# Kernel optimization log

Hardware: AMD Instinct MI355X
Metric: run time of the kernel (lower is better)

The kernel has to match this reference:

```python
import jax, jax.numpy as jnp
import numpy as np

B, S, D = 2, 2048, 1024
H = 16
HS = D // H  # head_size = 64
SCALE = HS ** 0.5


def setup_inputs() -> dict:
    key = jax.random.key(0)
    ks = jax.random.split(key, 7)
    std = 1.0 / np.sqrt(D)
    return {
        "x": jax.random.normal(ks[0], (B, S, D), dtype=jnp.float32),
        "Wq": jax.random.normal(ks[1], (D, D), dtype=jnp.float32) * std,
        "bq": jax.random.normal(ks[2], (D,), dtype=jnp.float32) * std,
        "Wk": jax.random.normal(ks[3], (D, D), dtype=jnp.float32) * std,
        "bk": jax.random.normal(ks[4], (D,), dtype=jnp.float32) * std,
        "Wv": jax.random.normal(ks[5], (D, D), dtype=jnp.float32) * std,
        "bv": jax.random.normal(ks[6], (D,), dtype=jnp.float32) * std,
    }


def reference(x, Wq, bq, Wk, bk, Wv, bv):
    bs, seq, _ = x.shape
    # QKV projections (torch Linear: x @ W.T + b)
    Q = (x @ Wq.T + bq).reshape(bs, seq, H, HS)
    K = (x @ Wk.T + bk).reshape(bs, seq, H, HS)
    V = (x @ Wv.T + bv).reshape(bs, seq, H, HS)
    # scores[b,h,q,k] = Q . K / scale
    scores = jnp.einsum("bqhd,bkhd->bhqk", Q, K) / SCALE
    # causal mask: disallow k > q
    causal = jnp.triu(jnp.ones((seq, seq), dtype=bool), k=1)
    scores = jnp.where(causal, -jnp.inf, scores)
    probs = jax.nn.softmax(scores, axis=-1)
    att = jnp.einsum("bhqk,bkhd->bqhd", probs, V)
    return att.reshape(bs, seq, H * HS)
```

## Files before the change

### kernel.cpp

```cpp
#include <hip/hip_runtime.h>

typedef unsigned short ushort_t;
typedef __bf16 bf16x8 __attribute__((ext_vector_type(8)));
typedef unsigned short ushortx8 __attribute__((ext_vector_type(8)));
typedef unsigned short ushortx4 __attribute__((ext_vector_type(4)));
typedef unsigned int uintx4 __attribute__((ext_vector_type(4)));
typedef float floatx4 __attribute__((ext_vector_type(4)));

__device__ inline void load16_lds(const ushort_t* g, ushort_t* l) {
  __builtin_amdgcn_global_load_lds(
      (__attribute__((address_space(1))) void*)(g),
      (__attribute__((address_space(3))) void*)(l),
      16, 0, 0);
}

__device__ inline float bf2f(ushort_t u) {
  unsigned int v = ((unsigned int)u) << 16;
  return __builtin_bit_cast(float, v);
}

__device__ inline ushort_t f2bf(float f) {
  unsigned int u = __builtin_bit_cast(unsigned int, f);
  u += 0x7fffu + ((u >> 16) & 1u);
  return (ushort_t)(u >> 16);
}

__device__ inline bf16x8 ldfrag(const ushort_t* p) {
  return __builtin_bit_cast(bf16x8, *(const ushortx8*)p);
}

__device__ inline bool sniff_f32(const ushort_t* x, int lane_off) {
  float v = fabsf(bf2f(x[lane_off]));
  bool big = !(v < 1e4f);
  return __ballot(big) != 0ull;
}

__global__ __launch_bounds__(256) void convert_all(
    const void* __restrict__ x,
    const void* __restrict__ wq, const void* __restrict__ wk, const void* __restrict__ wv,
    const void* __restrict__ bq, const void* __restrict__ bk, const void* __restrict__ bv,
    ushort_t* __restrict__ xb, ushort_t* __restrict__ wqb,
    ushort_t* __restrict__ wkb, ushort_t* __restrict__ wvb,
    float* __restrict__ biasf, int* __restrict__ flag)
{
  const bool f32 = sniff_f32((const ushort_t*)x, (int)(threadIdx.x & 63));
  const int seg = blockIdx.y;
  if (seg == 4) {
    if (blockIdx.x == 0 && threadIdx.x == 0) *flag = f32 ? 1 : 0;
    const int i = blockIdx.x * 256 + threadIdx.x;
    if (i >= 1024) return;
    const void* bs[3] = {bq, bk, bv};
#pragma unroll
    for (int k = 0; k < 3; ++k)
      biasf[k * 1024 + i] = f32 ? ((const float*)bs[k])[i] : bf2f(((const ushort_t*)bs[k])[i]);
    return;
  }
  const void* src = (seg == 0) ? x : (seg == 1) ? wq : (seg == 2) ? wk : wv;
  ushort_t* dst   = (seg == 0) ? xb : (seg == 1) ? wqb : (seg == 2) ? wkb : wvb;
  const int n = (seg == 0) ? 4194304 : 1048576;
  const int i = (blockIdx.x * 256 + threadIdx.x) * 8;
  if (i >= n) return;
  if (f32) {
    const float* s = (const float*)src + i;
    ushortx8 o;
#pragma unroll
    for (int j = 0; j < 8; ++j) o[j] = f2bf(s[j]);
    *(ushortx8*)(dst + i) = o;
  } else {
    *(ushortx8*)(dst + i) = *(const ushortx8*)((const ushort_t*)src + i);
  }
}

__global__ __launch_bounds__(256, 2) void qkv_gemm(
    const ushort_t* __restrict__ x,
    const ushort_t* __restrict__ Wq, const ushort_t* __restrict__ Wk,
    const ushort_t* __restrict__ Wv, const float* __restrict__ biasf,
    ushort_t* __restrict__ Qo, ushort_t* __restrict__ Ko, ushort_t* __restrict__ Vt)
{
  __shared__ __attribute__((aligned(16))) ushort_t As[128 * 32];
  __shared__ __attribute__((aligned(16))) ushort_t Bs[128 * 32];

  const int which = blockIdx.z;
  const ushort_t* W = (which == 0) ? Wq : (which == 1) ? Wk : Wv;
  const float oscale = (which == 0) ? 0.18033688011112042f : 1.0f;

  const int n0 = blockIdx.x * 128;
  const int m0 = blockIdx.y * 128;

  const int tid  = threadIdx.x;
  const int wave = tid >> 6;
  const int lane = tid & 63;
  const int ln   = lane & 15;
  const int quad = lane >> 4;
  const int wm = (wave >> 1) * 64;
  const int wn = (wave & 1) * 64;

  floatx4 acc[4][4];
#pragma unroll
  for (int i = 0; i < 4; ++i)
#pragma unroll
    for (int j = 0; j < 4; ++j) acc[i][j] = floatx4{0.f, 0.f, 0.f, 0.f};

  const int c1 = tid, c2 = tid + 256;
  const ushort_t* ga1 = x + (m0 + (c1 >> 2)) * 1024 + (c1 & 3) * 8;
  const ushort_t* ga2 = x + (m0 + (c2 >> 2)) * 1024 + (c2 & 3) * 8;
  const ushort_t* gb1 = W + (n0 + (c1 >> 2)) * 1024 + (c1 & 3) * 8;
  const ushort_t* gb2 = W + (n0 + (c2 >> 2)) * 1024 + (c2 & 3) * 8;
  ushort_t* la1 = As + wave * 512;
  ushort_t* la2 = As + 2048 + wave * 512;
  ushort_t* lb1 = Bs + wave * 512;
  ushort_t* lb2 = Bs + 2048 + wave * 512;

  for (int kt = 0; kt < 1024; kt += 32) {
    __syncthreads();
    load16_lds(ga1 + kt, la1);
    load16_lds(ga2 + kt, la2);
    load16_lds(gb1 + kt, lb1);
    load16_lds(gb2 + kt, lb2);
    __syncthreads();

    bf16x8 af[4], bfr[4];
#pragma unroll
    for (int mi = 0; mi < 4; ++mi)
      af[mi] = ldfrag(As + (wm + mi * 16 + ln) * 32 + quad * 8);
#pragma unroll
    for (int ni = 0; ni < 4; ++ni)
      bfr[ni] = ldfrag(Bs + (wn + ni * 16 + ln) * 32 + quad * 8);
#pragma unroll
    for (int mi = 0; mi < 4; ++mi)
#pragma unroll
      for (int ni = 0; ni < 4; ++ni)
        acc[mi][ni] = __builtin_amdgcn_mfma_f32_16x16x32_bf16(af[mi], bfr[ni], acc[mi][ni], 0, 0, 0);
  }

  float bvv[4];
#pragma unroll
  for (int ni = 0; ni < 4; ++ni) bvv[ni] = biasf[which * 1024 + n0 + wn + ni * 16 + ln];

  if (which == 2) {
#pragma unroll
    for (int mi = 0; mi < 4; ++mi)
#pragma unroll
      for (int ni = 0; ni < 4; ++ni) {
        const int col = n0 + wn + ni * 16 + ln;
        const int row0 = m0 + wm + mi * 16 + quad * 4;
        const int b = row0 >> 11, s0 = row0 & 2047;
        const int h = col >> 6, hs = col & 63;
        ushortx4 pk;
#pragma unroll
        for (int r = 0; r < 4; ++r) pk[r] = f2bf(acc[mi][ni][r] + bvv[ni]);
        *(ushortx4*)(Vt + ((size_t)((b * 16 + h) * 64 + hs)) * 2048 + s0) = pk;
      }
  } else {
    ushort_t* out = (which == 0) ? Qo : Ko;
#pragma unroll
    for (int mi = 0; mi < 4; ++mi)
#pragma unroll
      for (int ni = 0; ni < 4; ++ni) {
        const int col = n0 + wn + ni * 16 + ln;
#pragma unroll
        for (int r = 0; r < 4; ++r) {
          const int row = m0 + wm + mi * 16 + quad * 4 + r;
          out[row * 1024 + col] = f2bf((acc[mi][ni][r] + bvv[ni]) * oscale);
        }
      }
  }
}

__global__ __launch_bounds__(128) void flash8(
    const ushort_t* __restrict__ Q, const ushort_t* __restrict__ Kx,
    const ushort_t* __restrict__ Vt, void* __restrict__ out,
    const int* __restrict__ flag)
{
  __shared__ __attribute__((aligned(16))) float Cb[64][68];
  __shared__ float lbuf[64][4];

  const bool f32o = (*flag != 0);
  const int tid  = threadIdx.x;
  const int wave = tid >> 6;
  const int lane = tid & 63;
  const int ln = lane & 15, quad = lane >> 4;

  const int idxA = (ln + 32 * (quad & 1)) * 4;
  const int idxB = idxA + 64;
  const bool hiq = (quad >> 1) != 0;

  const int i = blockIdx.x;
  const int xcd = i & 7, j = i >> 3;
  const int bh = xcd * 4 + (j & 3);
  const int cc = 31 - (j >> 2);
  const int b = bh >> 4, h = bh & 15;
  const int qw = cc * 64;
  const int ntiles = cc + 1;

  const ushort_t* kbase = Kx + ((size_t)b * 2048) * 1024 + h * 64;
  const ushort_t* vbase = Vt + (size_t)bh * 64 * 2048;

  bf16x8 qf[4][2];
#pragma unroll
  for (int bi = 0; bi < 4; ++bi)
#pragma unroll
    for (int ks = 0; ks < 2; ++ks)
      qf[bi][ks] = ldfrag(Q + (size_t)(b * 2048 + qw + bi * 16 + ln) * 1024 + h * 64 + ks * 32 + quad * 8);

  floatx4 ot[4][4];
#pragma unroll
  for (int ai = 0; ai < 4; ++ai)
#pragma unroll
    for (int bi = 0; bi < 4; ++bi) ot[ai][bi] = floatx4{0.f, 0.f, 0.f, 0.f};
  float li[4] = {0.f, 0.f, 0.f, 0.f};

  for (int t = wave; t < ntiles; t += 2) {
    const int kv0 = t * 64;
    const bool diag = (t == ntiles - 1);

    const ushort_t* kp = kbase + (size_t)(kv0 + ln) * 1024 + quad * 8;
    bf16x8 kf[4][2];
#pragma unroll
    for (int mi = 0; mi < 4; ++mi)
#pragma unroll
      for (int ks = 0; ks < 2; ++ks)
        kf[mi][ks] = ldfrag(kp + mi * 16 * 1024 + ks * 32);

    const ushort_t* vp = vbase + (size_t)ln * 2048 + kv0 + quad * 8;
    bf16x8 vf[4][2];
#pragma unroll
    for (int ai = 0; ai < 4; ++ai)
#pragma unroll
      for (int ks = 0; ks < 2; ++ks)
        vf[ai][ks] = ldfrag(vp + ai * 16 * 2048 + ks * 32);

#pragma unroll
    for (int bi = 0; bi < 4; ++bi) {
      floatx4 st[4];
#pragma unroll
      for (int mi = 0; mi < 4; ++mi) st[mi] = floatx4{0.f, 0.f, 0.f, 0.f};
#pragma unroll
      for (int mi = 0; mi < 4; ++mi) {
        st[mi] = __builtin_amdgcn_mfma_f32_16x16x32_bf16(kf[mi][0], qf[bi][0], st[mi], 0, 0, 0);
        st[mi] = __builtin_amdgcn_mfma_f32_16x16x32_bf16(kf[mi][1], qf[bi][1], st[mi], 0, 0, 0);
      }

      const int qrow = qw + bi * 16 + ln;
      float p[4][4];
      if (diag) {
#pragma unroll
        for (int mi = 0; mi < 4; ++mi)
#pragma unroll
          for (int r = 0; r < 4; ++r) {
            const int kv = kv0 + mi * 16 + quad * 4 + r;
            const float e = __builtin_amdgcn_exp2f(st[mi][r]);
            p[mi][r] = (kv > qrow) ? 0.f : e;
          }
      } else {
#pragma unroll
        for (int mi = 0; mi < 4; ++mi)
#pragma unroll
          for (int r = 0; r < 4; ++r) p[mi][r] = __builtin_amdgcn_exp2f(st[mi][r]);
      }

      unsigned d[4][2];
#pragma unroll
      for (int mi = 0; mi < 4; ++mi) {
        li[bi] += (p[mi][0] + p[mi][1]) + (p[mi][2] + p[mi][3]);
        d[mi][0] = __builtin_amdgcn_perm(
            __builtin_bit_cast(unsigned, p[mi][1]), __builtin_bit_cast(unsigned, p[mi][0]), 0x07060302u);
        d[mi][1] = __builtin_amdgcn_perm(
            __builtin_bit_cast(unsigned, p[mi][3]), __builtin_bit_cast(unsigned, p[mi][2]), 0x07060302u);
      }

      bf16x8 pb[2];
#pragma unroll
      for (int ks = 0; ks < 2; ++ks) {
        uintx4 w;
#pragma unroll
        for (int jj = 0; jj < 4; ++jj) {
          const int idx = (jj >> 1) ? idxB : idxA;
          const int lo = __builtin_amdgcn_ds_bpermute(idx, (int)d[2 * ks][jj & 1]);
          const int hi = __builtin_amdgcn_ds_bpermute(idx, (int)d[2 * ks + 1][jj & 1]);
          w[jj] = (unsigned)(hiq ? hi : lo);
        }
        pb[ks] = __builtin_bit_cast(bf16x8, w);
      }

#pragma unroll
      for (int ai = 0; ai < 4; ++ai) {
        ot[ai][bi] = __builtin_amdgcn_mfma_f32_16x16x32_bf16(vf[ai][0], pb[0], ot[ai][bi], 0, 0, 0);
        ot[ai][bi] = __builtin_amdgcn_mfma_f32_16x16x32_bf16(vf[ai][1], pb[1], ot[ai][bi], 0, 0, 0);
      }
    }
  }

  if (wave == 1) {
#pragma unroll
    for (int bi = 0; bi < 4; ++bi) {
#pragma unroll
      for (int ai = 0; ai < 4; ++ai)
        *(floatx4*)&Cb[bi * 16 + ln][ai * 16 + quad * 4] = ot[ai][bi];
      lbuf[bi * 16 + ln][quad] = 0.f;
    }
#pragma unroll
    for (int bi = 0; bi < 4; ++bi) lbuf[lane][bi] = li[bi];
  }
  __syncthreads();
  if (wave == 0) {
#pragma unroll
    for (int bi = 0; bi < 4; ++bi) {
#pragma unroll
      for (int ai = 0; ai < 4; ++ai) {
        const floatx4 o = *(const floatx4*)&Cb[bi * 16 + ln][ai * 16 + quad * 4];
#pragma unroll
        for (int r = 0; r < 4; ++r) ot[ai][bi][r] += o[r];
      }
      li[bi] += lbuf[lane][bi];
    }

#pragma unroll
    for (int bi = 0; bi < 4; ++bi) {
      li[bi] += __shfl_xor(li[bi], 16);
      li[bi] += __shfl_xor(li[bi], 32);
      const float inv = 1.0f / li[bi];
      const int qrow = qw + bi * 16 + ln;
      if (f32o) {
        float* of = (float*)out;
#pragma unroll
        for (int ai = 0; ai < 4; ++ai) {
          floatx4 o;
#pragma unroll
          for (int r = 0; r < 4; ++r) o[r] = ot[ai][bi][r] * inv;
          *(floatx4*)(of + (size_t)(b * 2048 + qrow) * 1024 + h * 64 + ai * 16 + quad * 4) = o;
        }
      } else {
        ushort_t* ob = (ushort_t*)out;
#pragma unroll
        for (int ai = 0; ai < 4; ++ai) {
          ushortx4 pk;
#pragma unroll
          for (int r = 0; r < 4; ++r) pk[r] = f2bf(ot[ai][bi][r] * inv);
          *(ushortx4*)(ob + (size_t)(b * 2048 + qrow) * 1024 + h * 64 + ai * 16 + quad * 4) = pk;
        }
      }
    }
  }
}

extern "C" void kernel_launch(void* const* d_in, const int* in_sizes, int n_in,
                              void* d_out, int out_size, void* d_ws, size_t ws_size,
                              hipStream_t stream) {
  char* w = (char*)d_ws;
  int* flag = (int*)w;
  size_t off = 256;
  ushort_t* xb  = (ushort_t*)(w + off); off += (size_t)4194304 * 2;
  ushort_t* wqb = (ushort_t*)(w + off); off += (size_t)1048576 * 2;
  ushort_t* wkb = (ushort_t*)(w + off); off += (size_t)1048576 * 2;
  ushort_t* wvb = (ushort_t*)(w + off); off += (size_t)1048576 * 2;
  float* biasf  = (float*)(w + off);    off += (size_t)3 * 1024 * 4;
  ushort_t* Qw  = (ushort_t*)(w + off); off += (size_t)4194304 * 2;
  ushort_t* Kw  = (ushort_t*)(w + off); off += (size_t)4194304 * 2;
  ushort_t* Vtw = (ushort_t*)(w + off);

  convert_all<<<dim3(2048, 5), 256, 0, stream>>>(
      d_in[0], d_in[1], d_in[3], d_in[5], d_in[2], d_in[4], d_in[6],
      xb, wqb, wkb, wvb, biasf, flag);
  qkv_gemm<<<dim3(8, 32, 3), 256, 0, stream>>>(xb, wqb, wkb, wvb, biasf, Qw, Kw, Vtw);
  flash8<<<1024, 128, 0, stream>>>(Qw, Kw, Vtw, d_out, flag);
}
```

Measured before the change: 161.3 us.

## Share double-buffered LDS K/V tiles across two query-block waves in flash kernel

The attention kernel now gives each 2-wave block 128 query rows (64 per wave) instead of splitting one 64-row block's KV range across two waves. K and V tiles are staged through double-buffered LDS, with the next tile's global loads issued into registers during compute. This removes the cross-wave reduction of partial outputs and halves global K/V traffic per query row. The cost is one barrier per KV tile and idle time for wave 0 on the final tile. The grid drops to 512 blocks with a new causal-balanced ordering.

```diff
diff --git a/kernel.cpp b/kernel.cpp
--- a/kernel.cpp
+++ b/kernel.cpp
@@ -167,13 +167,13 @@
   }
 }
 
-__global__ __launch_bounds__(128) void flash8(
+__global__ __launch_bounds__(128) void flash9(
     const ushort_t* __restrict__ Q, const ushort_t* __restrict__ Kx,
     const ushort_t* __restrict__ Vt, void* __restrict__ out,
     const int* __restrict__ flag)
 {
-  __shared__ __attribute__((aligned(16))) float Cb[64][68];
-  __shared__ float lbuf[64][4];
+  __shared__ __attribute__((aligned(16))) ushort_t sK[2][64 * 72];
+  __shared__ __attribute__((aligned(16))) ushort_t sV[2][64 * 72];
 
   const bool f32o = (*flag != 0);
   const int tid  = threadIdx.x;
@@ -185,13 +185,18 @@
   const int idxB = idxA + 64;
   const bool hiq = (quad >> 1) != 0;
 
+  const int rl   = (lane & 15) + 16 * ((lane >> 5) & 1);
+  const int hsel = (lane >> 4) & 1;
+
   const int i = blockIdx.x;
-  const int xcd = i & 7, j = i >> 3;
-  const int bh = xcd * 4 + (j & 3);
-  const int cc = 31 - (j >> 2);
+  const int s = (i < 256) ? (i >> 5) : ((i - 256) >> 5);
+  const int c = (i < 256) ? (15 - s) : s;
+  const int bhi = i & 31;
+  const int bh = (bhi & 7) * 4 + (bhi >> 3);
   const int b = bh >> 4, h = bh & 15;
-  const int qw = cc * 64;
-  const int ntiles = cc + 1;
+  const int qw = c * 128 + wave * 64;
+  const int ntiles = 2 * c + 2;
+  const int mytiles = 2 * c + wave;
 
   const ushort_t* kbase = Kx + ((size_t)b * 2048) * 1024 + h * 64;
   const ushort_t* vbase = Vt + (size_t)bh * 64 * 2048;
@@ -210,135 +215,140 @@
     for (int bi = 0; bi < 4; ++bi) ot[ai][bi] = floatx4{0.f, 0.f, 0.f, 0.f};
   float li[4] = {0.f, 0.f, 0.f, 0.f};
 
-  for (int t = wave; t < ntiles; t += 2) {
+  uintx4 stgK[4], stgV[4];
+  {
+    const ushort_t* kg = kbase + (size_t)(0 + 32 * wave + rl) * 1024 + hsel * 32;
+    const ushort_t* vg = vbase + (size_t)(32 * wave + rl) * 2048 + 0 + hsel * 32;
+#pragma unroll
+    for (int c16 = 0; c16 < 4; ++c16) {
+      stgK[c16] = *(const uintx4*)(kg + c16 * 8);
+      stgV[c16] = *(const uintx4*)(vg + c16 * 8);
+    }
+  }
+
+  for (int t = 0; t < ntiles; ++t) {
     const int kv0 = t * 64;
-    const bool diag = (t == ntiles - 1);
-
-    const ushort_t* kp = kbase + (size_t)(kv0 + ln) * 1024 + quad * 8;
-    bf16x8 kf[4][2];
-#pragma unroll
-    for (int mi = 0; mi < 4; ++mi)
-#pragma unroll
-      for (int ks = 0; ks < 2; ++ks)
-        kf[mi][ks] = ldfrag(kp + mi * 16 * 1024 + ks * 32);
-
-    const ushort_t* vp = vbase + (size_t)ln * 2048 + kv0 + quad * 8;
-    bf16x8 vf[4][2];
-#pragma unroll
-    for (int ai = 0; ai < 4; ++ai)
-#pragma unroll
-      for (int ks = 0; ks < 2; ++ks)
-        vf[ai][ks] = ldfrag(vp + ai * 16 * 2048 + ks * 32);
-
-#pragma unroll
-    for (int bi = 0; bi < 4; ++bi) {
-      floatx4 st[4];
-#pragma unroll
-      for (int mi = 0; mi < 4; ++mi) st[mi] = floatx4{0.f, 0.f, 0.f, 0.f};
-#pragma unroll
-      for (int mi = 0; mi < 4; ++mi) {
-        st[mi] = __builtin_amdgcn_mfma_f32_16x16x32_bf16(kf[mi][0], qf[bi][0], st[mi], 0, 0, 0);
-        st[mi] = __builtin_amdgcn_mfma_f32_16x16x32_bf16(kf[mi][1], qf[bi][1], st[mi], 0, 0, 0);
-      }
-
-      const int qrow = qw + bi * 16 + ln;
-      float p[4][4];
-      if (diag) {
-#pragma unroll
-        for (int mi = 0; mi < 4; ++mi)
-#pragma unroll
-          for (int r = 0; r < 4; ++r) {
-            const int kv = kv0 + mi * 16 + quad * 4 + r;
-            const float e = __builtin_amdgcn_exp2f(st[mi][r]);
-            p[mi][r] = (kv > qrow) ? 0.f : e;
+    const int buf = t & 1;
+
+    {
+      ushort_t* wk = sK[buf] + (32 * wave + rl) * 72 + hsel * 32;
+      ushort_t* wv = sV[buf] + (32 * wave + rl) * 72 + hsel * 32;
+#pragma unroll
+      for (int c16 = 0; c16 < 4; ++c16) {
+        *(uintx4*)(wk + c16 * 8) = stgK[c16];
+        *(uintx4*)(wv + c16 * 8) = stgV[c16];
+      }
+    }
+    __syncthreads();
+
+    if (t + 1 < ntiles) {
+      const int kvn = (t + 1) * 64;
+      const ushort_t* kg = kbase + (size_t)(kvn + 32 * wave + rl) * 1024 + hsel * 32;
+      const ushort_t* vg = vbase + (size_t)(32 * wave + rl) * 2048 + kvn + hsel * 32;
+#pragma unroll
+      for (int c16 = 0; c16 < 4; ++c16) {
+        stgK[c16] = *(const uintx4*)(kg + c16 * 8);
+        stgV[c16] = *(const uintx4*)(vg + c16 * 8);
+      }
+    }
+
+    if (t <= mytiles) {
+      const bool diag = (t == mytiles);
+
+      bf16x8 kf[4][2], vf[4][2];
+#pragma unroll
+      for (int mi = 0; mi < 4; ++mi)
+#pragma unroll
+        for (int ks = 0; ks < 2; ++ks) {
+          kf[mi][ks] = ldfrag(sK[buf] + (mi * 16 + ln) * 72 + ks * 32 + quad * 8);
+          vf[mi][ks] = ldfrag(sV[buf] + (mi * 16 + ln) * 72 + ks * 32 + quad * 8);
+        }
+
+#pragma unroll
+      for (int bi = 0; bi < 4; ++bi) {
+        floatx4 st[4];
+#pragma unroll
+        for (int mi = 0; mi < 4; ++mi) st[mi] = floatx4{0.f, 0.f, 0.f, 0.f};
+#pragma unroll
+        for (int mi = 0; mi < 4; ++mi) {
+          st[mi] = __builtin_amdgcn_mfma_f32_16x16x32_bf16(kf[mi][0], qf[bi][0], st[mi], 0, 0, 0);
+          st[mi] = __builtin_amdgcn_mfma_f32_16x16x32_bf16(kf[mi][1], qf[bi][1], st[mi], 0, 0, 0);
+        }
+
+        const int qrow = qw + bi * 16 + ln;
+        float p[4][4];
+        if (diag) {
+#pragma unroll
+          for (int mi = 0; mi < 4; ++mi)
+#pragma unroll
+            for (int r = 0; r < 4; ++r) {
+              const int kv = kv0 + mi * 16 + quad * 4 + r;
+              const float e = __builtin_amdgcn_exp2f(st[mi][r]);
+              p[mi][r] = (kv > qrow) ? 0.f : e;
+            }
+        } else {
+#pragma unroll
+          for (int mi = 0; mi < 4; ++mi)
+#pragma unroll
+            for (int r = 0; r < 4; ++r) p[mi][r] = __builtin_amdgcn_exp2f(st[mi][r]);
+        }
+
+        unsigned d[4][2];
+#pragma unroll
+        for (int mi = 0; mi < 4; ++mi) {
+          li[bi] += (p[mi][0] + p[mi][1]) + (p[mi][2] + p[mi][3]);
+          d[mi][0] = __builtin_amdgcn_perm(
+              __builtin_bit_cast(unsigned, p[mi][1]), __builtin_bit_cast(unsigned, p[mi][0]), 0x07060302u);
+          d[mi][1] = __builtin_amdgcn_perm(
+              __builtin_bit_cast(unsigned, p[mi][3]), __builtin_bit_cast(unsigned, p[mi][2]), 0x07060302u);
+        }
+
+        bf16x8 pb[2];
+#pragma unroll
+        for (int ks = 0; ks < 2; ++ks) {
+          uintx4 w;
+#pragma unroll
+          for (int jj = 0; jj < 4; ++jj) {
+            const int idx = (jj >> 1) ? idxB : idxA;
+            const int lo = __builtin_amdgcn_ds_bpermute(idx, (int)d[2 * ks][jj & 1]);
+            const int hi = __builtin_amdgcn_ds_bpermute(idx, (int)d[2 * ks + 1][jj & 1]);
+            w[jj] = (unsigned)(hiq ? hi : lo);
           }
-      } else {
-#pragma unroll
-        for (int mi = 0; mi < 4; ++mi)
-#pragma unroll
-          for (int r = 0; r < 4; ++r) p[mi][r] = __builtin_amdgcn_exp2f(st[mi][r]);
-      }
-
-      unsigned d[4][2];
-#pragma unroll
-      for (int mi = 0; mi < 4; ++mi) {
-        li[bi] += (p[mi][0] + p[mi][1]) + (p[mi][2] + p[mi][3]);
-        d[mi][0] = __builtin_amdgcn_perm(
-            __builtin_bit_cast(unsigned, p[mi][1]), __builtin_bit_cast(unsigned, p[mi][0]), 0x07060302u);
-        d[mi][1] = __builtin_amdgcn_perm(
-            __builtin_bit_cast(unsigned, p[mi][3]), __builtin_bit_cast(unsigned, p[mi][2]), 0x07060302u);
-      }
-
-      bf16x8 pb[2];
-#pragma unroll
-      for (int ks = 0; ks < 2; ++ks) {
-        uintx4 w;
-#pragma unroll
-        for (int jj = 0; jj < 4; ++jj) {
-          const int idx = (jj >> 1) ? idxB : idxA;
-          const int lo = __builtin_amdgcn_ds_bpermute(idx, (int)d[2 * ks][jj & 1]);
-          const int hi = __builtin_amdgcn_ds_bpermute(idx, (int)d[2 * ks + 1][jj & 1]);
-          w[jj] = (unsigned)(hiq ? hi : lo);
-        }
-        pb[ks] = __builtin_bit_cast(bf16x8, w);
-      }
-
+          pb[ks] = __builtin_bit_cast(bf16x8, w);
+        }
+
+#pragma unroll
+        for (int ai = 0; ai < 4; ++ai) {
+          ot[ai][bi] = __builtin_amdgcn_mfma_f32_16x16x32_bf16(vf[ai][0], pb[0], ot[ai][bi], 0, 0, 0);
+          ot[ai][bi] = __builtin_amdgcn_mfma_f32_16x16x32_bf16(vf[ai][1], pb[1], ot[ai][bi], 0, 0, 0);
+        }
+      }
+    }
+  }
+
+#pragma unroll
+  for (int bi = 0; bi < 4; ++bi) {
+    li[bi] += __shfl_xor(li[bi], 16);
+    li[bi] += __shfl_xor(li[bi], 32);
+    const float inv = 1.0f / li[bi];
+    const int qrow = qw + bi * 16 + ln;
+    if (f32o) {
+      float* of = (float*)out;
 #pragma unroll
       for (int ai = 0; ai < 4; ++ai) {
-        ot[ai][bi] = __builtin_amdgcn_mfma_f32_16x16x32_bf16(vf[ai][0], pb[0], ot[ai][bi], 0, 0, 0);
-        ot[ai][bi] = __builtin_amdgcn_mfma_f32_16x16x32_bf16(vf[ai][1], pb[1], ot[ai][bi], 0, 0, 0);
-      }
-    }
-  }
-
-  if (wave == 1) {
-#pragma unroll
-    for (int bi = 0; bi < 4; ++bi) {
-#pragma unroll
-      for (int ai = 0; ai < 4; ++ai)
-        *(floatx4*)&Cb[bi * 16 + ln][ai * 16 + quad * 4] = ot[ai][bi];
-      lbuf[bi * 16 + ln][quad] = 0.f;
-    }
-#pragma unroll
-    for (int bi = 0; bi < 4; ++bi) lbuf[lane][bi] = li[bi];
-  }
-  __syncthreads();
-  if (wave == 0) {
-#pragma unroll
-    for (int bi = 0; bi < 4; ++bi) {
+        floatx4 o;
+#pragma unroll
+        for (int r = 0; r < 4; ++r) o[r] = ot[ai][bi][r] * inv;
+        *(floatx4*)(of + (size_t)(b * 2048 + qrow) * 1024 + h * 64 + ai * 16 + quad * 4) = o;
+      }
+    } else {
+      ushort_t* ob = (ushort_t*)out;
 #pragma unroll
       for (int ai = 0; ai < 4; ++ai) {
-        const floatx4 o = *(const floatx4*)&Cb[bi * 16 + ln][ai * 16 + quad * 4];
-#pragma unroll
-        for (int r = 0; r < 4; ++r) ot[ai][bi][r] += o[r];
-      }
-      li[bi] += lbuf[lane][bi];
-    }
-
-#pragma unroll
-    for (int bi = 0; bi < 4; ++bi) {
-      li[bi] += __shfl_xor(li[bi], 16);
-      li[bi] += __shfl_xor(li[bi], 32);
-      const float inv = 1.0f / li[bi];
-      const int qrow = qw + bi * 16 + ln;
-      if (f32o) {
-        float* of = (float*)out;
-#pragma unroll
-        for (int ai = 0; ai < 4; ++ai) {
-          floatx4 o;
-#pragma unroll
-          for (int r = 0; r < 4; ++r) o[r] = ot[ai][bi][r] * inv;
-          *(floatx4*)(of + (size_t)(b * 2048 + qrow) * 1024 + h * 64 + ai * 16 + quad * 4) = o;
-        }
-      } else {
-        ushort_t* ob = (ushort_t*)out;
-#pragma unroll
-        for (int ai = 0; ai < 4; ++ai) {
-          ushortx4 pk;
-#pragma unroll
-          for (int r = 0; r < 4; ++r) pk[r] = f2bf(ot[ai][bi][r] * inv);
-          *(ushortx4*)(ob + (size_t)(b * 2048 + qrow) * 1024 + h * 64 + ai * 16 + quad * 4) = pk;
-        }
+        ushortx4 pk;
+#pragma unroll
+        for (int r = 0; r < 4; ++r) pk[r] = f2bf(ot[ai][bi][r] * inv);
+        *(ushortx4*)(ob + (size_t)(b * 2048 + qrow) * 1024 + h * 64 + ai * 16 + quad * 4) = pk;
       }
     }
   }
@@ -363,5 +373,5 @@
       d_in[0], d_in[1], d_in[3], d_in[5], d_in[2], d_in[4], d_in[6],
       xb, wqb, wkb, wvb, biasf, flag);
   qkv_gemm<<<dim3(8, 32, 3), 256, 0, stream>>>(xb, wqb, wkb, wvb, biasf, Qw, Kw, Vtw);
-  flash8<<<1024, 128, 0, stream>>>(Qw, Kw, Vtw, d_out, flag);
-}
+  flash9<<<512, 128, 0, stream>>>(Qw, Kw, Vtw, d_out, flag);
+}
```

After: 194.8 us. 20.8% more time.

## Pair causal query chunks per block and split KV tiles across four waves

Applied to the files above, without the earlier changes.

Each block now processes two 64-row query chunks in sequence, a long one (31-pr) and a short one (pr), so every block does the same amount of causal work. The grid is halved to 512 blocks. Blocks grow to 256 threads, with KV tiles strided across four waves instead of two. Partial outputs are combined through a two-level shared-memory tree reduction. This targets load imbalance and tail effects from uneven causal chunk sizes, at the cost of more barriers and fewer, larger blocks.

```diff
diff --git a/kernel.cpp b/kernel.cpp
--- a/kernel.cpp
+++ b/kernel.cpp
@@ -167,13 +167,14 @@
   }
 }
 
-__global__ __launch_bounds__(128) void flash8(
+__global__ __launch_bounds__(256) void flash10(
     const ushort_t* __restrict__ Q, const ushort_t* __restrict__ Kx,
     const ushort_t* __restrict__ Vt, void* __restrict__ out,
     const int* __restrict__ flag)
 {
-  __shared__ __attribute__((aligned(16))) float Cb[64][68];
-  __shared__ float lbuf[64][4];
+  __shared__ __attribute__((aligned(16))) float CbA[64][68];
+  __shared__ __attribute__((aligned(16))) float CbB[64][68];
+  __shared__ float lbA[64][4], lbB[64][4];
 
   const bool f32o = (*flag != 0);
   const int tid  = threadIdx.x;
@@ -188,156 +189,201 @@
   const int i = blockIdx.x;
   const int xcd = i & 7, j = i >> 3;
   const int bh = xcd * 4 + (j & 3);
-  const int cc = 31 - (j >> 2);
+  const int pr = j >> 2;
   const int b = bh >> 4, h = bh & 15;
-  const int qw = cc * 64;
-  const int ntiles = cc + 1;
 
   const ushort_t* kbase = Kx + ((size_t)b * 2048) * 1024 + h * 64;
   const ushort_t* vbase = Vt + (size_t)bh * 64 * 2048;
 
-  bf16x8 qf[4][2];
-#pragma unroll
-  for (int bi = 0; bi < 4; ++bi)
-#pragma unroll
-    for (int ks = 0; ks < 2; ++ks)
-      qf[bi][ks] = ldfrag(Q + (size_t)(b * 2048 + qw + bi * 16 + ln) * 1024 + h * 64 + ks * 32 + quad * 8);
-
-  floatx4 ot[4][4];
-#pragma unroll
-  for (int ai = 0; ai < 4; ++ai)
-#pragma unroll
-    for (int bi = 0; bi < 4; ++bi) ot[ai][bi] = floatx4{0.f, 0.f, 0.f, 0.f};
-  float li[4] = {0.f, 0.f, 0.f, 0.f};
-
-  for (int t = wave; t < ntiles; t += 2) {
-    const int kv0 = t * 64;
-    const bool diag = (t == ntiles - 1);
-
-    const ushort_t* kp = kbase + (size_t)(kv0 + ln) * 1024 + quad * 8;
-    bf16x8 kf[4][2];
-#pragma unroll
-    for (int mi = 0; mi < 4; ++mi)
+  for (int phase = 0; phase < 2; ++phase) {
+    const int c = phase ? pr : (31 - pr);
+    const int qw = c * 64;
+    const int ntiles = c + 1;
+
+    bf16x8 qf[4][2];
+#pragma unroll
+    for (int bi = 0; bi < 4; ++bi)
 #pragma unroll
       for (int ks = 0; ks < 2; ++ks)
-        kf[mi][ks] = ldfrag(kp + mi * 16 * 1024 + ks * 32);
-
-    const ushort_t* vp = vbase + (size_t)ln * 2048 + kv0 + quad * 8;
-    bf16x8 vf[4][2];
+        qf[bi][ks] = ldfrag(Q + (size_t)(b * 2048 + qw + bi * 16 + ln) * 1024 + h * 64 + ks * 32 + quad * 8);
+
+    floatx4 ot[4][4];
 #pragma unroll
     for (int ai = 0; ai < 4; ++ai)
 #pragma unroll
-      for (int ks = 0; ks < 2; ++ks)
-        vf[ai][ks] = ldfrag(vp + ai * 16 * 2048 + ks * 32);
-
-#pragma unroll
-    for (int bi = 0; bi < 4; ++bi) {
-      floatx4 st[4];
-#pragma unroll
-      for (int mi = 0; mi < 4; ++mi) st[mi] = floatx4{0.f, 0.f, 0.f, 0.f};
-#pragma unroll
-      for (int mi = 0; mi < 4; ++mi) {
-        st[mi] = __builtin_amdgcn_mfma_f32_16x16x32_bf16(kf[mi][0], qf[bi][0], st[mi], 0, 0, 0);
-        st[mi] = __builtin_amdgcn_mfma_f32_16x16x32_bf16(kf[mi][1], qf[bi][1], st[mi], 0, 0, 0);
-      }
-
-      const int qrow = qw + bi * 16 + ln;
-      float p[4][4];
-      if (diag) {
-#pragma unroll
-        for (int mi = 0; mi < 4; ++mi)
-#pragma unroll
-          for (int r = 0; r < 4; ++r) {
-            const int kv = kv0 + mi * 16 + quad * 4 + r;
-            const float e = __builtin_amdgcn_exp2f(st[mi][r]);
-            p[mi][r] = (kv > qrow) ? 0.f : e;
+      for (int bi = 0; bi < 4; ++bi) ot[ai][bi] = floatx4{0.f, 0.f, 0.f, 0.f};
+    float li[4] = {0.f, 0.f, 0.f, 0.f};
+
+    for (int t = wave; t < ntiles; t += 4) {
+      const int kv0 = t * 64;
+      const bool diag = (t == ntiles - 1);
+
+      const ushort_t* kp = kbase + (size_t)(kv0 + ln) * 1024 + quad * 8;
+      bf16x8 kf[4][2];
+#pragma unroll
+      for (int mi = 0; mi < 4; ++mi)
+#pragma unroll
+        for (int ks = 0; ks < 2; ++ks)
+          kf[mi][ks] = ldfrag(kp + mi * 16 * 1024 + ks * 32);
+
+      const ushort_t* vp = vbase + (size_t)ln * 2048 + kv0 + quad * 8;
+      bf16x8 vf[4][2];
+#pragma unroll
+      for (int ai = 0; ai < 4; ++ai)
+#pragma unroll
+        for (int ks = 0; ks < 2; ++ks)
+          vf[ai][ks] = ldfrag(vp + ai * 16 * 2048 + ks * 32);
+
+#pragma unroll
+      for (int bi = 0; bi < 4; ++bi) {
+        floatx4 st[4];
+#pragma unroll
+        for (int mi = 0; mi < 4; ++mi) st[mi] = floatx4{0.f, 0.f, 0.f, 0.f};
+#pragma unroll
+        for (int mi = 0; mi < 4; ++mi) {
+          st[mi] = __builtin_amdgcn_mfma_f32_16x16x32_bf16(kf[mi][0], qf[bi][0], st[mi], 0, 0, 0);
+          st[mi] = __builtin_amdgcn_mfma_f32_16x16x32_bf16(kf[mi][1], qf[bi][1], st[mi], 0, 0, 0);
+        }
+
+        const int qrow = qw + bi * 16 + ln;
+        float p[4][4];
+        if (diag) {
+#pragma unroll
+          for (int mi = 0; mi < 4; ++mi)
+#pragma unroll
+            for (int r = 0; r < 4; ++r) {
+              const int kv = kv0 + mi * 16 + quad * 4 + r;
+              const float e = __builtin_amdgcn_exp2f(st[mi][r]);
+              p[mi][r] = (kv > qrow) ? 0.f : e;
+            }
+        } else {
+#pragma unroll
+          for (int mi = 0; mi < 4; ++mi)
+#pragma unroll
+            for (int r = 0; r < 4; ++r) p[mi][r] = __builtin_amdgcn_exp2f(st[mi][r]);
+        }
+
+        unsigned d[4][2];
+#pragma unroll
+        for (int mi = 0; mi < 4; ++mi) {
+          li[bi] += (p[mi][0] + p[mi][1]) + (p[mi][2] + p[mi][3]);
+          d[mi][0] = __builtin_amdgcn_perm(
+              __builtin_bit_cast(unsigned, p[mi][1]), __builtin_bit_cast(unsigned, p[mi][0]), 0x07060302u);
+          d[mi][1] = __builtin_amdgcn_perm(
+              __builtin_bit_cast(unsigned, p[mi][3]), __builtin_bit_cast(unsigned, p[mi][2]), 0x07060302u);
+        }
+
+        bf16x8 pb[2];
+#pragma unroll
+        for (int ks = 0; ks < 2; ++ks) {
+          uintx4 w;
+#pragma unroll
+          for (int jj = 0; jj < 4; ++jj) {
+            const int idx = (jj >> 1) ? idxB : idxA;
+            const int lo = __builtin_amdgcn_ds_bpermute(idx, (int)d[2 * ks][jj & 1]);
+            const int hi = __builtin_amdgcn_ds_bpermute(idx, (int)d[2 * ks + 1][jj & 1]);
+            w[jj] = (unsigned)(hiq ? hi : lo);
           }
-      } else {
-#pragma unroll
-        for (int mi = 0; mi < 4; ++mi)
-#pragma unroll
-          for (int r = 0; r < 4; ++r) p[mi][r] = __builtin_amdgcn_exp2f(st[mi][r]);
-      }
-
-      unsigned d[4][2];
-#pragma unroll
-      for (int mi = 0; mi < 4; ++mi) {
-        li[bi] += (p[mi][0] + p[mi][1]) + (p[mi][2] + p[mi][3]);
-        d[mi][0] = __builtin_amdgcn_perm(
-            __builtin_bit_cast(unsigned, p[mi][1]), __builtin_bit_cast(unsigned, p[mi][0]), 0x07060302u);
-        d[mi][1] = __builtin_amdgcn_perm(
-            __builtin_bit_cast(unsigned, p[mi][3]), __builtin_bit_cast(unsigned, p[mi][2]), 0x07060302u);
-      }
-
-      bf16x8 pb[2];
-#pragma unroll
-      for (int ks = 0; ks < 2; ++ks) {
-        uintx4 w;
-#pragma unroll
-        for (int jj = 0; jj < 4; ++jj) {
-          const int idx = (jj >> 1) ? idxB : idxA;
-          const int lo = __builtin_amdgcn_ds_bpermute(idx, (int)d[2 * ks][jj & 1]);
-          const int hi = __builtin_amdgcn_ds_bpermute(idx, (int)d[2 * ks + 1][jj & 1]);
-          w[jj] = (unsigned)(hiq ? hi : lo);
-        }
-        pb[ks] = __builtin_bit_cast(bf16x8, w);
-      }
-
-#pragma unroll
-      for (int ai = 0; ai < 4; ++ai) {
-        ot[ai][bi] = __builtin_amdgcn_mfma_f32_16x16x32_bf16(vf[ai][0], pb[0], ot[ai][bi], 0, 0, 0);
-        ot[ai][bi] = __builtin_amdgcn_mfma_f32_16x16x32_bf16(vf[ai][1], pb[1], ot[ai][bi], 0, 0, 0);
+          pb[ks] = __builtin_bit_cast(bf16x8, w);
+        }
+
+#pragma unroll
+        for (int ai = 0; ai < 4; ++ai) {
+          ot[ai][bi] = __builtin_amdgcn_mfma_f32_16x16x32_bf16(vf[ai][0], pb[0], ot[ai][bi], 0, 0, 0);
+          ot[ai][bi] = __builtin_amdgcn_mfma_f32_16x16x32_bf16(vf[ai][1], pb[1], ot[ai][bi], 0, 0, 0);
+        }
       }
     }
-  }
-
-  if (wave == 1) {
-#pragma unroll
-    for (int bi = 0; bi < 4; ++bi) {
-#pragma unroll
-      for (int ai = 0; ai < 4; ++ai)
-        *(floatx4*)&Cb[bi * 16 + ln][ai * 16 + quad * 4] = ot[ai][bi];
-      lbuf[bi * 16 + ln][quad] = 0.f;
+
+    __syncthreads();
+    if (wave == 1) {
+#pragma unroll
+      for (int bi = 0; bi < 4; ++bi) {
+#pragma unroll
+        for (int ai = 0; ai < 4; ++ai)
+          *(floatx4*)&CbA[bi * 16 + ln][ai * 16 + quad * 4] = ot[ai][bi];
+        lbA[lane][bi] = li[bi];
+      }
+    } else if (wave == 3) {
+#pragma unroll
+      for (int bi = 0; bi < 4; ++bi) {
+#pragma unroll
+        for (int ai = 0; ai < 4; ++ai)
+          *(floatx4*)&CbB[bi * 16 + ln][ai * 16 + quad * 4] = ot[ai][bi];
+        lbB[lane][bi] = li[bi];
+      }
     }
-#pragma unroll
-    for (int bi = 0; bi < 4; ++bi) lbuf[lane][bi] = li[bi];
-  }
-  __syncthreads();
-  if (wave == 0) {
-#pragma unroll
-    for (int bi = 0; bi < 4; ++bi) {
-#pragma unroll
-      for (int ai = 0; ai < 4; ++ai) {
-        const floatx4 o = *(const floatx4*)&Cb[bi * 16 + ln][ai * 16 + quad * 4];
-#pragma unroll
-        for (int r = 0; r < 4; ++r) ot[ai][bi][r] += o[r];
-      }
-      li[bi] += lbuf[lane][bi];
+    __syncthreads();
+    if (wave == 0) {
+#pragma unroll
+      for (int bi = 0; bi < 4; ++bi) {
+#pragma unroll
+        for (int ai = 0; ai < 4; ++ai) {
+          const floatx4 o = *(const floatx4*)&CbA[bi * 16 + ln][ai * 16 + quad * 4];
+#pragma unroll
+          for (int r = 0; r < 4; ++r) ot[ai][bi][r] += o[r];
+        }
+        li[bi] += lbA[lane][bi];
+      }
+    } else if (wave == 2) {
+#pragma unroll
+      for (int bi = 0; bi < 4; ++bi) {
+#pragma unroll
+        for (int ai = 0; ai < 4; ++ai) {
+          const floatx4 o = *(const floatx4*)&CbB[bi * 16 + ln][ai * 16 + quad * 4];
+#pragma unroll
+          for (int r = 0; r < 4; ++r) ot[ai][bi][r] += o[r];
+        }
+        li[bi] += lbB[lane][bi];
+      }
     }
-
-#pragma unroll
-    for (int bi = 0; bi < 4; ++bi) {
-      li[bi] += __shfl_xor(li[bi], 16);
-      li[bi] += __shfl_xor(li[bi], 32);
-      const float inv = 1.0f / li[bi];
-      const int qrow = qw + bi * 16 + ln;
-      if (f32o) {
-        float* of = (float*)out;
+    __syncthreads();
+    if (wave == 2) {
+#pragma unroll
+      for (int bi = 0; bi < 4; ++bi) {
+#pragma unroll
+        for (int ai = 0; ai < 4; ++ai)
+          *(floatx4*)&CbA[bi * 16 + ln][ai * 16 + quad * 4] = ot[ai][bi];
+        lbA[lane][bi] = li[bi];
+      }
+    }
+    __syncthreads();
+    if (wave == 0) {
+#pragma unroll
+      for (int bi = 0; bi < 4; ++bi) {
 #pragma unroll
         for (int ai = 0; ai < 4; ++ai) {
-          floatx4 o;
-#pragma unroll
-          for (int r = 0; r < 4; ++r) o[r] = ot[ai][bi][r] * inv;
-          *(floatx4*)(of + (size_t)(b * 2048 + qrow) * 1024 + h * 64 + ai * 16 + quad * 4) = o;
-        }
-      } else {
-        ushort_t* ob = (ushort_t*)out;
-#pragma unroll
-        for (int ai = 0; ai < 4; ++ai) {
-          ushortx4 pk;
-#pragma unroll
-          for (int r = 0; r < 4; ++r) pk[r] = f2bf(ot[ai][bi][r] * inv);
-          *(ushortx4*)(ob + (size_t)(b * 2048 + qrow) * 1024 + h * 64 + ai * 16 + quad * 4) = pk;
+          const floatx4 o = *(const floatx4*)&CbA[bi * 16 + ln][ai * 16 + quad * 4];
+#pragma unroll
+          for (int r = 0; r < 4; ++r) ot[ai][bi][r] += o[r];
+        }
+        li[bi] += lbA[lane][bi];
+      }
+
+#pragma unroll
+      for (int bi = 0; bi < 4; ++bi) {
+        li[bi] += __shfl_xor(li[bi], 16);
+        li[bi] += __shfl_xor(li[bi], 32);
+        const float inv = 1.0f / li[bi];
+        const int qrow = qw + bi * 16 + ln;
+        if (f32o) {
+          float* of = (float*)out;
+#pragma unroll
+          for (int ai = 0; ai < 4; ++ai) {
+            floatx4 o;
+#pragma unroll
+            for (int r = 0; r < 4; ++r) o[r] = ot[ai][bi][r] * inv;
+            *(floatx4*)(of + (size_t)(b * 2048 + qrow) * 1024 + h * 64 + ai * 16 + quad * 4) = o;
+          }
+        } else {
+          ushort_t* ob = (ushort_t*)out;
+#pragma unroll
+          for (int ai = 0; ai < 4; ++ai) {
+            ushortx4 pk;
+#pragma unroll
+            for (int r = 0; r < 4; ++r) pk[r] = f2bf(ot[ai][bi][r] * inv);
+            *(ushortx4*)(ob + (size_t)(b * 2048 + qrow) * 1024 + h * 64 + ai * 16 + quad * 4) = pk;
+          }
         }
       }
     }
@@ -363,5 +409,5 @@
       d_in[0], d_in[1], d_in[3], d_in[5], d_in[2], d_in[4], d_in[6],
       xb, wqb, wkb, wvb, biasf, flag);
   qkv_gemm<<<dim3(8, 32, 3), 256, 0, stream>>>(xb, wqb, wkb, wvb, biasf, Qw, Kw, Vtw);
-  flash8<<<1024, 128, 0, stream>>>(Qw, Kw, Vtw, d_out, flag);
-}
+  flash10<<<512, 256, 0, stream>>>(Qw, Kw, Vtw, d_out, flag);
+}
```

After: 171.1 us. 6.1% more time.
